# Kernel tuning notes

Hardware: AMD Instinct MI355X
Metric: run time of the kernel (lower is better)

The kernel has to match this reference:

```python
import jax, jax.numpy as jnp
import numpy as np

N = 100000      # nodes
E = 3200000     # edges (avg degree 32)
F_IN = 512      # node features
H = 256         # hidden width (channels[0])
C = 64          # num_classes
K = 10          # APPNP steps
ALPHA = 0.1     # teleport prob


def setup_inputs() -> dict:
    key = jax.random.key(0)
    k1, k2, k3, k4 = jax.random.split(key, 4)
    x = jax.random.normal(k1, (N, F_IN), dtype=jnp.float32)
    edge_index = jax.random.randint(k2, (2, E), 0, N, dtype=jnp.int32)
    W1 = jax.random.normal(k3, (F_IN, H), dtype=jnp.float32) * (1.0 / np.sqrt(F_IN))
    b1 = jnp.zeros((H,), dtype=jnp.float32)
    W2 = jax.random.normal(k4, (H, C), dtype=jnp.float32) * (1.0 / np.sqrt(H))
    b2 = jnp.zeros((C,), dtype=jnp.float32)
    return {"x": x, "edge_index": edge_index, "W1": W1, "b1": b1, "W2": W2, "b2": b2}


def reference(x, edge_index, W1, b1, W2, b2):
    # MLP encoder (dropout is identity at eval time)
    h = jax.nn.relu(x @ W1 + b1) @ W2 + b2  # [N, C]

    # GCN normalization with added self-loops (PyG APPNP default)
    loops = jnp.arange(N, dtype=edge_index.dtype)
    row = jnp.concatenate([edge_index[0], loops])  # source
    col = jnp.concatenate([edge_index[1], loops])  # target
    deg = jax.ops.segment_sum(jnp.ones_like(col, dtype=h.dtype), col, num_segments=N)
    dinv = jnp.where(deg > 0, jax.lax.rsqrt(deg), 0.0)
    norm = (dinv[row] * dinv[col])[:, None]  # [E+N, 1]

    # APPNP: z_{k+1} = (1-alpha) * A_hat z_k + alpha * h
    z = h
    for _ in range(K):
        msg = z[row] * norm                                   # gather + scale
        agg = jax.ops.segment_sum(msg, col, num_segments=N)   # scatter-add
        z = (1.0 - ALPHA) * agg + ALPHA * h

    return jax.nn.log_softmax(z, axis=1)
```

## Files before the change

kernel.cpp:

```cpp
#include <hip/hip_runtime.h>
#include <hip/hip_bf16.h>

#define F_IN 512
#define H_DIM 256
#define C_DIM 64
#define K_STEPS 10
#define ALPHA 0.1f

typedef __attribute__((ext_vector_type(8))) short bf16x8;
typedef __attribute__((ext_vector_type(4))) float f32x4;

static __device__ __forceinline__ ushort f2bf(float f) {
    __hip_bfloat16 b = __float2bfloat16(f);
    return *(ushort*)&b;
}
static __device__ __forceinline__ float bflo(unsigned int w) {
    union { unsigned int i; float f; } v; v.i = w << 16; return v.f;
}
static __device__ __forceinline__ float bfhi(unsigned int w) {
    union { unsigned int i; float f; } v; v.i = w & 0xffff0000u; return v.f;
}

#define ACC8(u) do { \
    acc[0] += bflo(u.x); acc[1] += bfhi(u.x); \
    acc[2] += bflo(u.y); acc[3] += bfhi(u.y); \
    acc[4] += bflo(u.z); acc[5] += bfhi(u.z); \
    acc[6] += bflo(u.w); acc[7] += bfhi(u.w); } while (0)

#define GLOAD_LDS16(gp, lp) __builtin_amdgcn_global_load_lds( \
    (const __attribute__((address_space(1))) unsigned int*)(gp), \
    (__attribute__((address_space(3))) unsigned int*)(lp), 16, 0, 0)

__global__ void prep_kernel(const float* __restrict__ W1, ushort* __restrict__ W1p,
                            const float* __restrict__ W2, ushort* __restrict__ W2p,
                            int* __restrict__ cnt, int n)
{
    const int o = blockIdx.x * 256 + threadIdx.x;
    {
        const int j = o & 7;
        const int l = (o >> 3) & 63;
        const int b = o >> 9;
        const int f = b & 15, ks = b >> 4;
        const int k = ks * 32 + (l >> 4) * 8 + j;
        const int col = f * 16 + (l & 15);
        W1p[o] = f2bf(W1[k * H_DIM + col]);
    }
    if (o < 16384) {
        const int j = o & 7;
        const int l = (o >> 3) & 63;
        const int b = o >> 9;
        const int f = b & 3, kk = b >> 2;
        const int k = kk * 32 + (l >> 4) * 8 + j;
        const int col = f * 16 + (l & 15);
        W2p[o] = f2bf(W2[k * C_DIM + col]);
    }
    if (o < n) cnt[o] = 0;
}

__global__ void rank_kernel(const int* __restrict__ col, int* __restrict__ cnt,
                            int* __restrict__ rank, int e)
{
    const int i0 = (blockIdx.x * 256 + threadIdx.x) * 8;
    if (i0 + 7 < e) {
        const int4 ca = *(const int4*)&col[i0];
        const int4 cb = *(const int4*)&col[i0 + 4];
        const int r0 = atomicAdd(&cnt[ca.x], 1);
        const int r1 = atomicAdd(&cnt[ca.y], 1);
        const int r2 = atomicAdd(&cnt[ca.z], 1);
        const int r3 = atomicAdd(&cnt[ca.w], 1);
        const int r4 = atomicAdd(&cnt[cb.x], 1);
        const int r5 = atomicAdd(&cnt[cb.y], 1);
        const int r6 = atomicAdd(&cnt[cb.z], 1);
        const int r7 = atomicAdd(&cnt[cb.w], 1);
        *(int4*)&rank[i0]     = make_int4(r0, r1, r2, r3);
        *(int4*)&rank[i0 + 4] = make_int4(r4, r5, r6, r7);
    } else {
        for (int i = i0; i < e; ++i) rank[i] = atomicAdd(&cnt[col[i]], 1);
    }
}

__global__ __launch_bounds__(256) void scan1_kernel(
    const int* __restrict__ cnt, int* __restrict__ rowptr, int* __restrict__ sums,
    float* __restrict__ dinv, int n)
{
    __shared__ int lds[256];
    const int t = threadIdx.x;
    const int base = blockIdx.x * 1024 + t * 4;
    int v[4];
    #pragma unroll
    for (int j = 0; j < 4; ++j) v[j] = (base + j < n) ? cnt[base + j] : 0;
    const int tsum = v[0] + v[1] + v[2] + v[3];
    lds[t] = tsum;
    __syncthreads();
    for (int o = 1; o < 256; o <<= 1) {
        const int add = (t >= o) ? lds[t - o] : 0;
        __syncthreads();
        lds[t] += add;
        __syncthreads();
    }
    int run = lds[t] - tsum;
    #pragma unroll
    for (int j = 0; j < 4; ++j) {
        if (base + j < n) {
            rowptr[base + j] = run;
            dinv[base + j] = rsqrtf((float)v[j] + 1.0f);
        }
        run += v[j];
    }
    if (t == 255) sums[blockIdx.x] = lds[255];
}

__global__ __launch_bounds__(128) void scan2_kernel(int* __restrict__ sums, int nc)
{
    __shared__ int lds[128];
    const int t = threadIdx.x;
    const int v = (t < nc) ? sums[t] : 0;
    lds[t] = v;
    __syncthreads();
    for (int o = 1; o < 128; o <<= 1) {
        const int add = (t >= o) ? lds[t - o] : 0;
        __syncthreads();
        lds[t] += add;
        __syncthreads();
    }
    if (t < nc) sums[t] = lds[t] - v;
}

__global__ void scan3_kernel(int* __restrict__ rowptr, const int* __restrict__ sums, int n, int e)
{
    int i = blockIdx.x * 256 + threadIdx.x;
    if (i < n) rowptr[i] += sums[i >> 10];
    else if (i == n) rowptr[n] = e;
}

__global__ void fill_kernel(const int* __restrict__ row, const int* __restrict__ col,
                            const int* __restrict__ rowptr, const int* __restrict__ rank,
                            int* __restrict__ csr_src, int e)
{
    const int i0 = (blockIdx.x * 256 + threadIdx.x) * 8;
    if (i0 + 7 < e) {
        const int4 ca  = *(const int4*)&col[i0];
        const int4 cb  = *(const int4*)&col[i0 + 4];
        const int4 ka  = *(const int4*)&rank[i0];
        const int4 kb  = *(const int4*)&rank[i0 + 4];
        const int4 ra  = *(const int4*)&row[i0];
        const int4 rb  = *(const int4*)&row[i0 + 4];
        csr_src[rowptr[ca.x] + ka.x] = ra.x;
        csr_src[rowptr[ca.y] + ka.y] = ra.y;
        csr_src[rowptr[ca.z] + ka.z] = ra.z;
        csr_src[rowptr[ca.w] + ka.w] = ra.w;
        csr_src[rowptr[cb.x] + kb.x] = rb.x;
        csr_src[rowptr[cb.y] + kb.y] = rb.y;
        csr_src[rowptr[cb.z] + kb.z] = rb.z;
        csr_src[rowptr[cb.w] + kb.w] = rb.w;
    } else {
        for (int i = i0; i < e; ++i) csr_src[rowptr[col[i]] + rank[i]] = row[i];
    }
}

__global__ __launch_bounds__(256) void mlp_mfma_kernel(
    const float* __restrict__ x,
    const ushort* __restrict__ W1p, const float* __restrict__ b1,
    const ushort* __restrict__ W2p, const float* __restrict__ b2,
    const float* __restrict__ dinv,
    ushort* __restrict__ ah, ushort* __restrict__ zs, int n)
{
    __shared__ __align__(16) char smem[32768];

    const int t = threadIdx.x;
    const int lane = t & 63;
    const int wv = t >> 6;
    const int ln15 = lane & 15;
    const int hi = lane >> 4;
    const long row0 = (long)blockIdx.x * 64 + wv * 16;

    long arow = row0 + ln15;
    if (arow > (long)n - 1) arow = n - 1;
    const float4* xp = (const float4*)(x + arow * F_IN);

    f32x4 acc[16];
    #pragma unroll
    for (int f = 0; f < 16; ++f) acc[f] = (f32x4){0.f, 0.f, 0.f, 0.f};

    {
        const char* g = (const char*)(W1p);
        char* l = smem;
        #pragma unroll
        for (int j = 0; j < 4; ++j)
            GLOAD_LDS16(g + j * 4096 + wv * 1024 + lane * 16,
                        l + j * 4096 + wv * 1024);
    }
    __syncthreads();

    for (int ks = 0; ks < 16; ++ks) {
        if (ks < 15) {
            const char* g = (const char*)(W1p + (size_t)(ks + 1) * 8192);
            char* l = smem + ((ks + 1) & 1) * 16384;
            #pragma unroll
            for (int j = 0; j < 4; ++j)
                GLOAD_LDS16(g + j * 4096 + wv * 1024 + lane * 16,
                            l + j * 4096 + wv * 1024);
        }
        const float4 a0 = xp[ks * 8 + hi * 2];
        const float4 a1 = xp[ks * 8 + hi * 2 + 1];
        bf16x8 af;
        af[0] = (short)f2bf(a0.x); af[1] = (short)f2bf(a0.y);
        af[2] = (short)f2bf(a0.z); af[3] = (short)f2bf(a0.w);
        af[4] = (short)f2bf(a1.x); af[5] = (short)f2bf(a1.y);
        af[6] = (short)f2bf(a1.z); af[7] = (short)f2bf(a1.w);
        const ushort* wb = (const ushort*)(smem + (ks & 1) * 16384) + lane * 8;
        #pragma unroll
        for (int f = 0; f < 16; ++f) {
            const bf16x8 bfv = *(const bf16x8*)(wb + f * 512);
            acc[f] = __builtin_amdgcn_mfma_f32_16x16x32_bf16(af, bfv, acc[f], 0, 0, 0);
        }
        __syncthreads();
    }

    char* hreg = smem + wv * 8192;
    #pragma unroll
    for (int f = 0; f < 16; ++f) {
        const int col = f * 16 + ln15;
        const float bias = b1[col];
        #pragma unroll
        for (int v = 0; v < 4; ++v) {
            const int r = hi * 4 + v;
            float val = acc[f][v] + bias;
            val = val > 0.f ? val : 0.f;
            const int pos = (r * 256 + col) * 2;
            *(short*)(hreg + (pos ^ ((r & 7) << 4))) = (short)f2bf(val);
        }
    }

    f32x4 acc2[4];
    #pragma unroll
    for (int f = 0; f < 4; ++f) acc2[f] = (f32x4){0.f, 0.f, 0.f, 0.f};
    #pragma unroll
    for (int kk = 0; kk < 8; ++kk) {
        const int pos = (ln15 * 256 + kk * 32 + hi * 8) * 2;
        const bf16x8 a2 = *(const bf16x8*)(hreg + (pos ^ ((ln15 & 7) << 4)));
        #pragma unroll
        for (int f = 0; f < 4; ++f) {
            const bf16x8 b2f = *(const bf16x8*)&W2p[(kk * 4 + f) * 512 + lane * 8];
            acc2[f] = __builtin_amdgcn_mfma_f32_16x16x32_bf16(a2, b2f, acc2[f], 0, 0, 0);
        }
    }

    float di4[4];
    #pragma unroll
    for (int v = 0; v < 4; ++v) {
        const long r = row0 + hi * 4 + v;
        di4[v] = (r < n) ? dinv[r] : 0.f;
    }
    #pragma unroll
    for (int f = 0; f < 4; ++f) {
        const int col = f * 16 + ln15;
        const float bias = b2[col];
        #pragma unroll
        for (int v = 0; v < 4; ++v) {
            const long r = row0 + hi * 4 + v;
            if (r < n) {
                const float val = acc2[f][v] + bias;
                ah[r * C_DIM + col] = f2bf(ALPHA * val);
                zs[r * C_DIM + col] = f2bf(val * di4[v]);
            }
        }
    }
}

__global__ __launch_bounds__(256) void gather8_kernel(
    const int* __restrict__ rowptr, const int* __restrict__ csr_src,
    const float* __restrict__ dinv, const ushort* __restrict__ ah,
    const ushort* __restrict__ zs_in, ushort* __restrict__ zs_out,
    float* __restrict__ out, int n, int final_it)
{
    const int node = (blockIdx.x * 256 + threadIdx.x) >> 6;
    if (node >= n) return;
    const int lane = threadIdx.x & 63;
    const int s = lane >> 3;
    const int cg = lane & 7;

    const int p0 = rowptr[node];
    const int p1 = rowptr[node + 1];

    float acc[8];
    #pragma unroll
    for (int c = 0; c < 8; ++c) acc[c] = 0.f;

    if (s == 0) {
        const uint4 u = *(const uint4*)&zs_in[(long)node * C_DIM + cg * 8];
        ACC8(u);
    }

    for (int p = (p0 & ~3) + s * 4; p < p1; p += 32) {
        const int4 iv = *(const int4*)&csr_src[p];
        const bool k0 = (p     >= p0) & (p     < p1);
        const bool k1 = (p + 1 >= p0) & (p + 1 < p1);
        const bool k2 = (p + 2 >= p0) & (p + 2 < p1);
        const bool k3 = (p + 3 >= p0) & (p + 3 < p1);
        const int i0 = k0 ? iv.x : 0;
        const int i1 = k1 ? iv.y : 0;
        const int i2 = k2 ? iv.z : 0;
        const int i3 = k3 ? iv.w : 0;
        const uint4 u0 = *(const uint4*)&zs_in[(long)i0 * C_DIM + cg * 8];
        const uint4 u1 = *(const uint4*)&zs_in[(long)i1 * C_DIM + cg * 8];
        const uint4 u2 = *(const uint4*)&zs_in[(long)i2 * C_DIM + cg * 8];
        const uint4 u3 = *(const uint4*)&zs_in[(long)i3 * C_DIM + cg * 8];
        if (k0) ACC8(u0);
        if (k1) ACC8(u1);
        if (k2) ACC8(u2);
        if (k3) ACC8(u3);
    }

    #pragma unroll
    for (int c = 0; c < 8; ++c) {
        acc[c] += __shfl_xor(acc[c], 8, 64);
        acc[c] += __shfl_xor(acc[c], 16, 64);
        acc[c] += __shfl_xor(acc[c], 32, 64);
    }

    if (s == 0) {
        const float di = dinv[node];
        const long off = (long)node * C_DIM + cg * 8;
        const uint4 ua = *(const uint4*)&ah[off];
        const float w = (1.0f - ALPHA) * di;
        float z[8];
        z[0] = w * acc[0] + bflo(ua.x);
        z[1] = w * acc[1] + bfhi(ua.x);
        z[2] = w * acc[2] + bflo(ua.y);
        z[3] = w * acc[3] + bfhi(ua.y);
        z[4] = w * acc[4] + bflo(ua.z);
        z[5] = w * acc[5] + bfhi(ua.z);
        z[6] = w * acc[6] + bflo(ua.w);
        z[7] = w * acc[7] + bfhi(ua.w);
        if (!final_it) {
            uint4 o;
            o.x = ((unsigned)f2bf(z[1] * di) << 16) | f2bf(z[0] * di);
            o.y = ((unsigned)f2bf(z[3] * di) << 16) | f2bf(z[2] * di);
            o.z = ((unsigned)f2bf(z[5] * di) << 16) | f2bf(z[4] * di);
            o.w = ((unsigned)f2bf(z[7] * di) << 16) | f2bf(z[6] * di);
            *(uint4*)&zs_out[off] = o;
        } else {
            float m = z[0];
            #pragma unroll
            for (int j = 1; j < 8; ++j) m = fmaxf(m, z[j]);
            m = fmaxf(m, __shfl_xor(m, 1, 64));
            m = fmaxf(m, __shfl_xor(m, 2, 64));
            m = fmaxf(m, __shfl_xor(m, 4, 64));
            float se = 0.f;
            #pragma unroll
            for (int j = 0; j < 8; ++j) se += expf(z[j] - m);
            se += __shfl_xor(se, 1, 64);
            se += __shfl_xor(se, 2, 64);
            se += __shfl_xor(se, 4, 64);
            const float ls = m + logf(se);
            *(float4*)&out[off]     = make_float4(z[0] - ls, z[1] - ls, z[2] - ls, z[3] - ls);
            *(float4*)&out[off + 4] = make_float4(z[4] - ls, z[5] - ls, z[6] - ls, z[7] - ls);
        }
    }
}

extern "C" void kernel_launch(void* const* d_in, const int* in_sizes, int n_in,
                              void* d_out, int out_size, void* d_ws, size_t ws_size,
                              hipStream_t stream)
{
    const float* x  = (const float*)d_in[0];
    const int* ei   = (const int*)d_in[1];
    const float* W1 = (const float*)d_in[2];
    const float* b1 = (const float*)d_in[3];
    const float* W2 = (const float*)d_in[4];
    const float* b2 = (const float*)d_in[5];
    float* out = (float*)d_out;

    const int N = in_sizes[0] / F_IN;
    const int E = in_sizes[1] / 2;
    const int* row = ei;
    const int* col = ei + E;

    ushort* ah     = (ushort*)d_ws;
    ushort* zs_a   = ah + (size_t)N * C_DIM;
    ushort* zs_b   = zs_a + (size_t)N * C_DIM;
    float*  dinv   = (float*)(zs_b + (size_t)N * C_DIM);
    int*    cnt    = (int*)(dinv + N);
    int*    rowptr = cnt + N;
    int*    rank   = rowptr + N + 16;
    int*    csr_src = rank + E;
    int*    sums   = csr_src + E + 4;
    ushort* W1p    = (ushort*)(sums + 128);
    ushort* W2p    = W1p + 131072;

    const int eblk8 = (E / 8 + 255) / 256;
    const int nchunks = (N + 1023) / 1024;

    prep_kernel<<<512, 256, 0, stream>>>(W1, W1p, W2, W2p, cnt, N);

    rank_kernel<<<eblk8, 256, 0, stream>>>(col, cnt, rank, E);
    scan1_kernel<<<nchunks, 256, 0, stream>>>(cnt, rowptr, sums, dinv, N);
    scan2_kernel<<<1, 128, 0, stream>>>(sums, nchunks);
    scan3_kernel<<<(N + 256) / 256, 256, 0, stream>>>(rowptr, sums, N, E);
    fill_kernel<<<eblk8, 256, 0, stream>>>(row, col, rowptr, rank, csr_src, E);

    mlp_mfma_kernel<<<(N + 63) / 64, 256, 0, stream>>>(x, W1p, b1, W2p, b2,
                                                       dinv, ah, zs_a, N);

    const int gblk = (N + 3) / 4;
    for (int it = 0; it < K_STEPS; ++it) {
        const ushort* in = (it & 1) ? zs_b : zs_a;
        ushort* outb     = (it & 1) ? zs_a : zs_b;
        gather8_kernel<<<gblk, 256, 0, stream>>>(rowptr, csr_src, dinv, ah,
                                                 in, outb, out, N,
                                                 it == K_STEPS - 1 ? 1 : 0);
    }
}
```

Measured before the change: 892.7 us.

## Fuse APPNP iterations into one cooperative persistent kernel with grid sync

Replaces the ten separate gather kernel launches with a single cooperative persistent kernel of 2048 blocks that loops over nodes with a grid stride and uses grid.sync between propagation steps. This removes per-iteration launch overhead and tail effects. It also changes the neighbor loop to load indices one at a time with a software-prefetched next batch, instead of aligned int4 loads with masking. The persistent grid lowers parallelism per step and adds the cost of grid-wide barriers. If the cooperative launch fails, it falls back to the old per-step launches.

```diff
diff --git a/kernel.cpp b/kernel.cpp
--- a/kernel.cpp
+++ b/kernel.cpp
@@ -1,5 +1,8 @@
 #include <hip/hip_runtime.h>
 #include <hip/hip_bf16.h>
+#include <hip/hip_cooperative_groups.h>
+
+namespace cg = cooperative_groups;
 
 #define F_IN 512
 #define H_DIM 256
@@ -268,18 +271,13 @@
     }
 }
 
-__global__ __launch_bounds__(256) void gather8_kernel(
+static __device__ __forceinline__ void gather_node(
+    int node, int s, int cg8,
     const int* __restrict__ rowptr, const int* __restrict__ csr_src,
     const float* __restrict__ dinv, const ushort* __restrict__ ah,
     const ushort* __restrict__ zs_in, ushort* __restrict__ zs_out,
-    float* __restrict__ out, int n, int final_it)
-{
-    const int node = (blockIdx.x * 256 + threadIdx.x) >> 6;
-    if (node >= n) return;
-    const int lane = threadIdx.x & 63;
-    const int s = lane >> 3;
-    const int cg = lane & 7;
-
+    float* __restrict__ out, bool final_it)
+{
     const int p0 = rowptr[node];
     const int p1 = rowptr[node + 1];
 
@@ -288,28 +286,33 @@
     for (int c = 0; c < 8; ++c) acc[c] = 0.f;
 
     if (s == 0) {
-        const uint4 u = *(const uint4*)&zs_in[(long)node * C_DIM + cg * 8];
+        const uint4 u = *(const uint4*)&zs_in[(long)node * C_DIM + cg8 * 8];
         ACC8(u);
     }
 
-    for (int p = (p0 & ~3) + s * 4; p < p1; p += 32) {
-        const int4 iv = *(const int4*)&csr_src[p];
-        const bool k0 = (p     >= p0) & (p     < p1);
-        const bool k1 = (p + 1 >= p0) & (p + 1 < p1);
-        const bool k2 = (p + 2 >= p0) & (p + 2 < p1);
-        const bool k3 = (p + 3 >= p0) & (p + 3 < p1);
-        const int i0 = k0 ? iv.x : 0;
-        const int i1 = k1 ? iv.y : 0;
-        const int i2 = k2 ? iv.z : 0;
-        const int i3 = k3 ? iv.w : 0;
-        const uint4 u0 = *(const uint4*)&zs_in[(long)i0 * C_DIM + cg * 8];
-        const uint4 u1 = *(const uint4*)&zs_in[(long)i1 * C_DIM + cg * 8];
-        const uint4 u2 = *(const uint4*)&zs_in[(long)i2 * C_DIM + cg * 8];
-        const uint4 u3 = *(const uint4*)&zs_in[(long)i3 * C_DIM + cg * 8];
-        if (k0) ACC8(u0);
-        if (k1) ACC8(u1);
-        if (k2) ACC8(u2);
-        if (k3) ACC8(u3);
+    if (p0 < p1) {
+        int p = p0 + s;
+        int c0 = (p      < p1) ? csr_src[p]      : -1;
+        int c1 = (p +  8 < p1) ? csr_src[p +  8] : -1;
+        int c2 = (p + 16 < p1) ? csr_src[p + 16] : -1;
+        int c3 = (p + 24 < p1) ? csr_src[p + 24] : -1;
+        while (c0 >= 0) {
+            uint4 u0, u1, u2, u3;
+            u0 = *(const uint4*)&zs_in[(long)c0 * C_DIM + cg8 * 8];
+            if (c1 >= 0) u1 = *(const uint4*)&zs_in[(long)c1 * C_DIM + cg8 * 8];
+            if (c2 >= 0) u2 = *(const uint4*)&zs_in[(long)c2 * C_DIM + cg8 * 8];
+            if (c3 >= 0) u3 = *(const uint4*)&zs_in[(long)c3 * C_DIM + cg8 * 8];
+            p += 32;
+            const int n0 = (p      < p1) ? csr_src[p]      : -1;
+            const int n1 = (p +  8 < p1) ? csr_src[p +  8] : -1;
+            const int n2 = (p + 16 < p1) ? csr_src[p + 16] : -1;
+            const int n3 = (p + 24 < p1) ? csr_src[p + 24] : -1;
+            ACC8(u0);
+            if (c1 >= 0) ACC8(u1);
+            if (c2 >= 0) ACC8(u2);
+            if (c3 >= 0) ACC8(u3);
+            c0 = n0; c1 = n1; c2 = n2; c3 = n3;
+        }
     }
 
     #pragma unroll
@@ -321,7 +324,7 @@
 
     if (s == 0) {
         const float di = dinv[node];
-        const long off = (long)node * C_DIM + cg * 8;
+        const long off = (long)node * C_DIM + cg8 * 8;
         const uint4 ua = *(const uint4*)&ah[off];
         const float w = (1.0f - ALPHA) * di;
         float z[8];
@@ -360,6 +363,42 @@
     }
 }
 
+__global__ __launch_bounds__(256, 8) void appnp_kernel(
+    const int* __restrict__ rowptr, const int* __restrict__ csr_src,
+    const float* __restrict__ dinv, const ushort* __restrict__ ah,
+    ushort* __restrict__ zs_a, ushort* __restrict__ zs_b,
+    float* __restrict__ out, int n)
+{
+    cg::grid_group grid = cg::this_grid();
+    const int lane = threadIdx.x & 63;
+    const int wv = threadIdx.x >> 6;
+    const int s = lane >> 3;
+    const int cg8 = lane & 7;
+    const int node0 = blockIdx.x * 4 + wv;
+    const int stride = gridDim.x * 4;
+
+    for (int it = 0; it < K_STEPS; ++it) {
+        const ushort* zin = (it & 1) ? zs_b : zs_a;
+        ushort* zout      = (it & 1) ? zs_a : zs_b;
+        const bool fin = (it == K_STEPS - 1);
+        for (int node = node0; node < n; node += stride)
+            gather_node(node, s, cg8, rowptr, csr_src, dinv, ah, zin, zout, out, fin);
+        grid.sync();
+    }
+}
+
+__global__ __launch_bounds__(256) void gather8_kernel(
+    const int* __restrict__ rowptr, const int* __restrict__ csr_src,
+    const float* __restrict__ dinv, const ushort* __restrict__ ah,
+    const ushort* __restrict__ zs_in, ushort* __restrict__ zs_out,
+    float* __restrict__ out, int n, int final_it)
+{
+    const int node = (blockIdx.x * 256 + threadIdx.x) >> 6;
+    if (node >= n) return;
+    gather_node(node, (threadIdx.x & 63) >> 3, threadIdx.x & 7,
+                rowptr, csr_src, dinv, ah, zs_in, zs_out, out, final_it != 0);
+}
+
 extern "C" void kernel_launch(void* const* d_in, const int* in_sizes, int n_in,
                               void* d_out, int out_size, void* d_ws, size_t ws_size,
                               hipStream_t stream)
@@ -403,12 +442,23 @@
     mlp_mfma_kernel<<<(N + 63) / 64, 256, 0, stream>>>(x, W1p, b1, W2p, b2,
                                                        dinv, ah, zs_a, N);
 
-    const int gblk = (N + 3) / 4;
-    for (int it = 0; it < K_STEPS; ++it) {
-        const ushort* in = (it & 1) ? zs_b : zs_a;
-        ushort* outb     = (it & 1) ? zs_a : zs_b;
-        gather8_kernel<<<gblk, 256, 0, stream>>>(rowptr, csr_src, dinv, ah,
-                                                 in, outb, out, N,
-                                                 it == K_STEPS - 1 ? 1 : 0);
-    }
-}
+    {
+        const int* rp = rowptr; const int* cs = csr_src;
+        const float* dv = dinv; const ushort* ahp = ah;
+        ushort* za = zs_a; ushort* zb = zs_b;
+        float* op = out; int nn = N;
+        void* args[] = {&rp, &cs, &dv, &ahp, &za, &zb, &op, &nn};
+        hipError_t err = hipLaunchCooperativeKernel(
+            (const void*)appnp_kernel, dim3(2048), dim3(256), args, 0, stream);
+        if (err != hipSuccess) {
+            const int gblk = (N + 3) / 4;
+            for (int it = 0; it < K_STEPS; ++it) {
+                const ushort* in = (it & 1) ? zs_b : zs_a;
+                ushort* outb     = (it & 1) ? zs_a : zs_b;
+                gather8_kernel<<<gblk, 256, 0, stream>>>(rowptr, csr_src, dinv, ah,
+                                                         in, outb, out, N,
+                                                         it == K_STEPS - 1 ? 1 : 0);
+            }
+        }
+    }
+}
```

After: 3.458 ms. 3.87x slower.

## Co-schedule MLP with rank atomics in one launch and software-pipeline gather index loads

Applied to the files above, without the earlier changes.

The MLP encoder and the degree-counting atomic rank pass now run in a single launch, with even blocks doing MLP tiles and odd blocks doing atomics, so the compute-bound and atomic-bound work can overlap. The MLP writes fp32 h to a new workspace buffer, and a small zsinit kernel later scales it by dinv and alpha into bf16. The gather loop now strides by 8 per sub-lane over exact edge ranges and prefetches the next four CSR indices before accumulating. The cost is an extra fp32 N×C write and read, one more launch, and an MLP kernel that has to carry the LDS allocation even in blocks that only do atomics.

```diff
diff --git a/kernel.cpp b/kernel.cpp
--- a/kernel.cpp
+++ b/kernel.cpp
@@ -57,25 +57,126 @@
     if (o < n) cnt[o] = 0;
 }
 
-__global__ void rank_kernel(const int* __restrict__ col, int* __restrict__ cnt,
-                            int* __restrict__ rank, int e)
-{
-    const int i0 = (blockIdx.x * 256 + threadIdx.x) * 8;
-    if (i0 + 7 < e) {
-        const int4 ca = *(const int4*)&col[i0];
-        const int4 cb = *(const int4*)&col[i0 + 4];
-        const int r0 = atomicAdd(&cnt[ca.x], 1);
-        const int r1 = atomicAdd(&cnt[ca.y], 1);
-        const int r2 = atomicAdd(&cnt[ca.z], 1);
-        const int r3 = atomicAdd(&cnt[ca.w], 1);
-        const int r4 = atomicAdd(&cnt[cb.x], 1);
-        const int r5 = atomicAdd(&cnt[cb.y], 1);
-        const int r6 = atomicAdd(&cnt[cb.z], 1);
-        const int r7 = atomicAdd(&cnt[cb.w], 1);
-        *(int4*)&rank[i0]     = make_int4(r0, r1, r2, r3);
-        *(int4*)&rank[i0 + 4] = make_int4(r4, r5, r6, r7);
-    } else {
-        for (int i = i0; i < e; ++i) rank[i] = atomicAdd(&cnt[col[i]], 1);
+__global__ __launch_bounds__(256) void mlp_rank_kernel(
+    const float* __restrict__ x,
+    const ushort* __restrict__ W1p, const float* __restrict__ b1,
+    const ushort* __restrict__ W2p, const float* __restrict__ b2,
+    float* __restrict__ hf, int n,
+    const int* __restrict__ col, int* __restrict__ cnt,
+    int* __restrict__ rank, int e)
+{
+    __shared__ __align__(16) char smem[32768];
+
+    if (blockIdx.x & 1) {
+        const int i0 = ((blockIdx.x >> 1) * 256 + threadIdx.x) * 8;
+        if (i0 + 7 < e) {
+            const int4 ca = *(const int4*)&col[i0];
+            const int4 cb = *(const int4*)&col[i0 + 4];
+            const int r0 = atomicAdd(&cnt[ca.x], 1);
+            const int r1 = atomicAdd(&cnt[ca.y], 1);
+            const int r2 = atomicAdd(&cnt[ca.z], 1);
+            const int r3 = atomicAdd(&cnt[ca.w], 1);
+            const int r4 = atomicAdd(&cnt[cb.x], 1);
+            const int r5 = atomicAdd(&cnt[cb.y], 1);
+            const int r6 = atomicAdd(&cnt[cb.z], 1);
+            const int r7 = atomicAdd(&cnt[cb.w], 1);
+            *(int4*)&rank[i0]     = make_int4(r0, r1, r2, r3);
+            *(int4*)&rank[i0 + 4] = make_int4(r4, r5, r6, r7);
+        } else if (i0 < e) {
+            for (int i = i0; i < e; ++i) rank[i] = atomicAdd(&cnt[col[i]], 1);
+        }
+        return;
+    }
+
+    const int bx = blockIdx.x >> 1;
+    const int t = threadIdx.x;
+    const int lane = t & 63;
+    const int wv = t >> 6;
+    const int ln15 = lane & 15;
+    const int hi = lane >> 4;
+    const long row0 = (long)bx * 64 + wv * 16;
+
+    long arow = row0 + ln15;
+    if (arow > (long)n - 1) arow = n - 1;
+    const float4* xp = (const float4*)(x + arow * F_IN);
+
+    f32x4 acc[16];
+    #pragma unroll
+    for (int f = 0; f < 16; ++f) acc[f] = (f32x4){0.f, 0.f, 0.f, 0.f};
+
+    {
+        const char* g = (const char*)(W1p);
+        char* l = smem;
+        #pragma unroll
+        for (int j = 0; j < 4; ++j)
+            GLOAD_LDS16(g + j * 4096 + wv * 1024 + lane * 16,
+                        l + j * 4096 + wv * 1024);
+    }
+    __syncthreads();
+
+    for (int ks = 0; ks < 16; ++ks) {
+        if (ks < 15) {
+            const char* g = (const char*)(W1p + (size_t)(ks + 1) * 8192);
+            char* l = smem + ((ks + 1) & 1) * 16384;
+            #pragma unroll
+            for (int j = 0; j < 4; ++j)
+                GLOAD_LDS16(g + j * 4096 + wv * 1024 + lane * 16,
+                            l + j * 4096 + wv * 1024);
+        }
+        const float4 a0 = xp[ks * 8 + hi * 2];
+        const float4 a1 = xp[ks * 8 + hi * 2 + 1];
+        bf16x8 af;
+        af[0] = (short)f2bf(a0.x); af[1] = (short)f2bf(a0.y);
+        af[2] = (short)f2bf(a0.z); af[3] = (short)f2bf(a0.w);
+        af[4] = (short)f2bf(a1.x); af[5] = (short)f2bf(a1.y);
+        af[6] = (short)f2bf(a1.z); af[7] = (short)f2bf(a1.w);
+        const ushort* wb = (const ushort*)(smem + (ks & 1) * 16384) + lane * 8;
+        #pragma unroll
+        for (int f = 0; f < 16; ++f) {
+            const bf16x8 bfv = *(const bf16x8*)(wb + f * 512);
+            acc[f] = __builtin_amdgcn_mfma_f32_16x16x32_bf16(af, bfv, acc[f], 0, 0, 0);
+        }
+        __syncthreads();
+    }
+
+    char* hreg = smem + wv * 8192;
+    #pragma unroll
+    for (int f = 0; f < 16; ++f) {
+        const int c = f * 16 + ln15;
+        const float bias = b1[c];
+        #pragma unroll
+        for (int v = 0; v < 4; ++v) {
+            const int r = hi * 4 + v;
+            float val = acc[f][v] + bias;
+            val = val > 0.f ? val : 0.f;
+            const int pos = (r * 256 + c) * 2;
+            *(short*)(hreg + (pos ^ ((r & 7) << 4))) = (short)f2bf(val);
+        }
+    }
+
+    f32x4 acc2[4];
+    #pragma unroll
+    for (int f = 0; f < 4; ++f) acc2[f] = (f32x4){0.f, 0.f, 0.f, 0.f};
+    #pragma unroll
+    for (int kk = 0; kk < 8; ++kk) {
+        const int pos = (ln15 * 256 + kk * 32 + hi * 8) * 2;
+        const bf16x8 a2 = *(const bf16x8*)(hreg + (pos ^ ((ln15 & 7) << 4)));
+        #pragma unroll
+        for (int f = 0; f < 4; ++f) {
+            const bf16x8 b2f = *(const bf16x8*)&W2p[(kk * 4 + f) * 512 + lane * 8];
+            acc2[f] = __builtin_amdgcn_mfma_f32_16x16x32_bf16(a2, b2f, acc2[f], 0, 0, 0);
+        }
+    }
+
+    #pragma unroll
+    for (int f = 0; f < 4; ++f) {
+        const int c = f * 16 + ln15;
+        const float bias = b2[c];
+        #pragma unroll
+        for (int v = 0; v < 4; ++v) {
+            const long r = row0 + hi * 4 + v;
+            if (r < n) hf[r * C_DIM + c] = acc2[f][v] + bias;
+        }
     }
 }
 
@@ -158,114 +259,27 @@
     }
 }
 
-__global__ __launch_bounds__(256) void mlp_mfma_kernel(
-    const float* __restrict__ x,
-    const ushort* __restrict__ W1p, const float* __restrict__ b1,
-    const ushort* __restrict__ W2p, const float* __restrict__ b2,
-    const float* __restrict__ dinv,
-    ushort* __restrict__ ah, ushort* __restrict__ zs, int n)
-{
-    __shared__ __align__(16) char smem[32768];
-
-    const int t = threadIdx.x;
-    const int lane = t & 63;
-    const int wv = t >> 6;
-    const int ln15 = lane & 15;
-    const int hi = lane >> 4;
-    const long row0 = (long)blockIdx.x * 64 + wv * 16;
-
-    long arow = row0 + ln15;
-    if (arow > (long)n - 1) arow = n - 1;
-    const float4* xp = (const float4*)(x + arow * F_IN);
-
-    f32x4 acc[16];
-    #pragma unroll
-    for (int f = 0; f < 16; ++f) acc[f] = (f32x4){0.f, 0.f, 0.f, 0.f};
-
-    {
-        const char* g = (const char*)(W1p);
-        char* l = smem;
-        #pragma unroll
-        for (int j = 0; j < 4; ++j)
-            GLOAD_LDS16(g + j * 4096 + wv * 1024 + lane * 16,
-                        l + j * 4096 + wv * 1024);
-    }
-    __syncthreads();
-
-    for (int ks = 0; ks < 16; ++ks) {
-        if (ks < 15) {
-            const char* g = (const char*)(W1p + (size_t)(ks + 1) * 8192);
-            char* l = smem + ((ks + 1) & 1) * 16384;
-            #pragma unroll
-            for (int j = 0; j < 4; ++j)
-                GLOAD_LDS16(g + j * 4096 + wv * 1024 + lane * 16,
-                            l + j * 4096 + wv * 1024);
-        }
-        const float4 a0 = xp[ks * 8 + hi * 2];
-        const float4 a1 = xp[ks * 8 + hi * 2 + 1];
-        bf16x8 af;
-        af[0] = (short)f2bf(a0.x); af[1] = (short)f2bf(a0.y);
-        af[2] = (short)f2bf(a0.z); af[3] = (short)f2bf(a0.w);
-        af[4] = (short)f2bf(a1.x); af[5] = (short)f2bf(a1.y);
-        af[6] = (short)f2bf(a1.z); af[7] = (short)f2bf(a1.w);
-        const ushort* wb = (const ushort*)(smem + (ks & 1) * 16384) + lane * 8;
-        #pragma unroll
-        for (int f = 0; f < 16; ++f) {
-            const bf16x8 bfv = *(const bf16x8*)(wb + f * 512);
-            acc[f] = __builtin_amdgcn_mfma_f32_16x16x32_bf16(af, bfv, acc[f], 0, 0, 0);
-        }
-        __syncthreads();
-    }
-
-    char* hreg = smem + wv * 8192;
-    #pragma unroll
-    for (int f = 0; f < 16; ++f) {
-        const int col = f * 16 + ln15;
-        const float bias = b1[col];
-        #pragma unroll
-        for (int v = 0; v < 4; ++v) {
-            const int r = hi * 4 + v;
-            float val = acc[f][v] + bias;
-            val = val > 0.f ? val : 0.f;
-            const int pos = (r * 256 + col) * 2;
-            *(short*)(hreg + (pos ^ ((r & 7) << 4))) = (short)f2bf(val);
-        }
-    }
-
-    f32x4 acc2[4];
-    #pragma unroll
-    for (int f = 0; f < 4; ++f) acc2[f] = (f32x4){0.f, 0.f, 0.f, 0.f};
-    #pragma unroll
-    for (int kk = 0; kk < 8; ++kk) {
-        const int pos = (ln15 * 256 + kk * 32 + hi * 8) * 2;
-        const bf16x8 a2 = *(const bf16x8*)(hreg + (pos ^ ((ln15 & 7) << 4)));
-        #pragma unroll
-        for (int f = 0; f < 4; ++f) {
-            const bf16x8 b2f = *(const bf16x8*)&W2p[(kk * 4 + f) * 512 + lane * 8];
-            acc2[f] = __builtin_amdgcn_mfma_f32_16x16x32_bf16(a2, b2f, acc2[f], 0, 0, 0);
-        }
-    }
-
-    float di4[4];
-    #pragma unroll
-    for (int v = 0; v < 4; ++v) {
-        const long r = row0 + hi * 4 + v;
-        di4[v] = (r < n) ? dinv[r] : 0.f;
-    }
-    #pragma unroll
-    for (int f = 0; f < 4; ++f) {
-        const int col = f * 16 + ln15;
-        const float bias = b2[col];
-        #pragma unroll
-        for (int v = 0; v < 4; ++v) {
-            const long r = row0 + hi * 4 + v;
-            if (r < n) {
-                const float val = acc2[f][v] + bias;
-                ah[r * C_DIM + col] = f2bf(ALPHA * val);
-                zs[r * C_DIM + col] = f2bf(val * di4[v]);
-            }
-        }
-    }
+__global__ void zsinit_kernel(const float* __restrict__ hf, const float* __restrict__ dinv,
+                              ushort* __restrict__ ah, ushort* __restrict__ zs, int n)
+{
+    const int i = blockIdx.x * 256 + threadIdx.x;
+    if (i >= n * 8) return;
+    const int node = i >> 3, part = i & 7;
+    const float di = dinv[node];
+    const long off = (long)node * C_DIM + part * 8;
+    const float4 a = *(const float4*)&hf[off];
+    const float4 b = *(const float4*)&hf[off + 4];
+    uint4 z, ua;
+    z.x = ((unsigned)f2bf(a.y * di) << 16) | f2bf(a.x * di);
+    z.y = ((unsigned)f2bf(a.w * di) << 16) | f2bf(a.z * di);
+    z.z = ((unsigned)f2bf(b.y * di) << 16) | f2bf(b.x * di);
+    z.w = ((unsigned)f2bf(b.w * di) << 16) | f2bf(b.z * di);
+    ua.x = ((unsigned)f2bf(a.y * ALPHA) << 16) | f2bf(a.x * ALPHA);
+    ua.y = ((unsigned)f2bf(a.w * ALPHA) << 16) | f2bf(a.z * ALPHA);
+    ua.z = ((unsigned)f2bf(b.y * ALPHA) << 16) | f2bf(b.x * ALPHA);
+    ua.w = ((unsigned)f2bf(b.w * ALPHA) << 16) | f2bf(b.z * ALPHA);
+    *(uint4*)&zs[off] = z;
+    *(uint4*)&ah[off] = ua;
 }
 
 __global__ __launch_bounds__(256) void gather8_kernel(
@@ -292,24 +306,29 @@
         ACC8(u);
     }
 
-    for (int p = (p0 & ~3) + s * 4; p < p1; p += 32) {
-        const int4 iv = *(const int4*)&csr_src[p];
-        const bool k0 = (p     >= p0) & (p     < p1);
-        const bool k1 = (p + 1 >= p0) & (p + 1 < p1);
-        const bool k2 = (p + 2 >= p0) & (p + 2 < p1);
-        const bool k3 = (p + 3 >= p0) & (p + 3 < p1);
-        const int i0 = k0 ? iv.x : 0;
-        const int i1 = k1 ? iv.y : 0;
-        const int i2 = k2 ? iv.z : 0;
-        const int i3 = k3 ? iv.w : 0;
-        const uint4 u0 = *(const uint4*)&zs_in[(long)i0 * C_DIM + cg * 8];
-        const uint4 u1 = *(const uint4*)&zs_in[(long)i1 * C_DIM + cg * 8];
-        const uint4 u2 = *(const uint4*)&zs_in[(long)i2 * C_DIM + cg * 8];
-        const uint4 u3 = *(const uint4*)&zs_in[(long)i3 * C_DIM + cg * 8];
-        if (k0) ACC8(u0);
-        if (k1) ACC8(u1);
-        if (k2) ACC8(u2);
-        if (k3) ACC8(u3);
+    if (p0 < p1) {
+        int p = p0 + s;
+        int c0 = (p      < p1) ? csr_src[p]      : -1;
+        int c1 = (p +  8 < p1) ? csr_src[p +  8] : -1;
+        int c2 = (p + 16 < p1) ? csr_src[p + 16] : -1;
+        int c3 = (p + 24 < p1) ? csr_src[p + 24] : -1;
+        while (c0 >= 0) {
+            uint4 u0, u1, u2, u3;
+            u0 = *(const uint4*)&zs_in[(long)c0 * C_DIM + cg * 8];
+            if (c1 >= 0) u1 = *(const uint4*)&zs_in[(long)c1 * C_DIM + cg * 8];
+            if (c2 >= 0) u2 = *(const uint4*)&zs_in[(long)c2 * C_DIM + cg * 8];
+            if (c3 >= 0) u3 = *(const uint4*)&zs_in[(long)c3 * C_DIM + cg * 8];
+            p += 32;
+            const int n0 = (p      < p1) ? csr_src[p]      : -1;
+            const int n1 = (p +  8 < p1) ? csr_src[p +  8] : -1;
+            const int n2 = (p + 16 < p1) ? csr_src[p + 16] : -1;
+            const int n3 = (p + 24 < p1) ? csr_src[p + 24] : -1;
+            ACC8(u0);
+            if (c1 >= 0) ACC8(u1);
+            if (c2 >= 0) ACC8(u2);
+            if (c3 >= 0) ACC8(u3);
+            c0 = n0; c1 = n1; c2 = n2; c3 = n3;
+        }
     }
 
     #pragma unroll
@@ -380,7 +399,8 @@
     ushort* ah     = (ushort*)d_ws;
     ushort* zs_a   = ah + (size_t)N * C_DIM;
     ushort* zs_b   = zs_a + (size_t)N * C_DIM;
-    float*  dinv   = (float*)(zs_b + (size_t)N * C_DIM);
+    float*  hf     = (float*)(zs_b + (size_t)N * C_DIM);
+    float*  dinv   = hf + (size_t)N * C_DIM;
     int*    cnt    = (int*)(dinv + N);
     int*    rowptr = cnt + N;
     int*    rank   = rowptr + N + 16;
@@ -389,19 +409,22 @@
     ushort* W1p    = (ushort*)(sums + 128);
     ushort* W2p    = W1p + 131072;
 
-    const int eblk8 = (E / 8 + 255) / 256;
+    const int mlp_blocks  = (N + 63) / 64;
+    const int rank_blocks = (E / 8 + 255) / 256;
+    const int fused_blocks = 2 * ((mlp_blocks > rank_blocks) ? mlp_blocks : rank_blocks);
     const int nchunks = (N + 1023) / 1024;
 
     prep_kernel<<<512, 256, 0, stream>>>(W1, W1p, W2, W2p, cnt, N);
 
-    rank_kernel<<<eblk8, 256, 0, stream>>>(col, cnt, rank, E);
+    mlp_rank_kernel<<<fused_blocks, 256, 0, stream>>>(x, W1p, b1, W2p, b2, hf, N,
+                                                      col, cnt, rank, E);
+
     scan1_kernel<<<nchunks, 256, 0, stream>>>(cnt, rowptr, sums, dinv, N);
     scan2_kernel<<<1, 128, 0, stream>>>(sums, nchunks);
     scan3_kernel<<<(N + 256) / 256, 256, 0, stream>>>(rowptr, sums, N, E);
-    fill_kernel<<<eblk8, 256, 0, stream>>>(row, col, rowptr, rank, csr_src, E);
-
-    mlp_mfma_kernel<<<(N + 63) / 64, 256, 0, stream>>>(x, W1p, b1, W2p, b2,
-                                                       dinv, ah, zs_a, N);
+    fill_kernel<<<(E / 8 + 255) / 256, 256, 0, stream>>>(row, col, rowptr, rank, csr_src, E);
+
+    zsinit_kernel<<<(N * 8 + 255) / 256, 256, 0, stream>>>(hf, dinv, ah, zs_a, N);
 
     const int gblk = (N + 3) / 4;
     for (int it = 0; it < K_STEPS; ++it) {
```

Measured after the change: 798.9 us. 10.5% less time.
